# Kernel tuning notes

Measured on AMD Instinct MI355X. Metric: run time of the kernel, lower is better.

The kernel has to match this reference:

```python
import jax, jax.numpy as jnp
import numpy as np

BN_EPS = 1e-5
L2_EPS = 1e-12


def setup_inputs() -> dict:
    key = jax.random.key(0)
    ks = jax.random.split(key, 4)
    N, C = 524288, 32          # total points, FCGF feature dim
    L = 32768                  # points per cloud (segment length), B = N // L = 16
    K1, K2, FC = 128, 512, 256 # K_MLP = [128, 512], FC = [256]

    def lin(k, out_d, in_d):
        return jax.random.normal(k, (out_d, in_d), jnp.float32) * (1.0 / np.sqrt(in_d))

    return {
        "x": jax.random.normal(ks[0], (N, C), jnp.float32),
        "w1": lin(ks[1], K1, C),   "b1": jnp.zeros((K1,), jnp.float32),
        "g1": jnp.ones((K1,), jnp.float32), "be1": jnp.zeros((K1,), jnp.float32),
        "w2": lin(ks[2], K2, K1),  "b2": jnp.zeros((K2,), jnp.float32),
        "g2": jnp.ones((K2,), jnp.float32), "be2": jnp.zeros((K2,), jnp.float32),
        "wf": lin(ks[3], FC, C * K2), "bf": jnp.zeros((FC,), jnp.float32),
        "gf": jnp.ones((FC,), jnp.float32), "bef": jnp.zeros((FC,), jnp.float32),
        "seg_len": L,
    }


def _bn(h, g, b):
    # BatchNorm1d in training mode: per-channel batch stats (biased var),
    # reduction over all non-channel dims (here axis 0).
    mu = h.mean(axis=0, keepdims=True)
    var = h.var(axis=0, keepdims=True)
    return (h - mu) * jax.lax.rsqrt(var + BN_EPS) * g + b


def reference(x, w1, b1, g1, be1, w2, b2, g2, be2, wf, bf, gf, bef, seg_len):
    N = x.shape[0]
    B = N // seg_len
    # pointwise Conv1d == per-point Linear; BN over all N points per channel
    h = jax.nn.relu(_bn(x @ w1.T + b1, g1, be1))      # [N, 128]
    att = jax.nn.relu(_bn(h @ w2.T + b2, g2, be2))    # [N, 512]
    att_b = att.reshape(B, seg_len, att.shape[-1])    # [B, L, 512]
    x_b = x.reshape(B, seg_len, x.shape[-1])          # [B, L, 32]
    # per-segment attention-weighted pooling: att_i^T @ x_i / n_i
    pooled = jnp.einsum("blk,blc->bkc", att_b, x_b) / seg_len  # [B, 512, 32]
    gp = att_b.sum(axis=1)                            # [B, 512]
    res = _bn(pooled.reshape(B, -1) @ wf.T + bf, gf, bef)       # [B, 256]
    # F.normalize(p=2, dim=1)
    nrm = jnp.linalg.norm(res, axis=1, keepdims=True)
    res = res / jnp.maximum(nrm, L2_EPS)
    lengths = jnp.full((B, 1), seg_len, dtype=jnp.int32)
    return (res, gp, lengths)
```

## Files before the change

kernel.cpp:

```cpp
#include <hip/hip_runtime.h>
#include <hip/hip_bf16.h>


#define SEGLEN 32768
#define BN_EPS 1e-5f
#define INV_N (1.0f/524288.0f)
#define INV_L (1.0f/32768.0f)

#define WS_BIG   0
#define WS_TMPG  8650752
#define WS_S1    8782848
#define WS_G     8783904
#define WS_W1F   8800416
#define WS_B1P   8802464
#define WS_W2F   8802592
#define WS_B2P   8835360
#define WS_PR    8835872
#define WS_TP    9098016

typedef __attribute__((ext_vector_type(8))) short bf16x8;
typedef __attribute__((ext_vector_type(4))) float f32x4;
#define MFMA(a,b,c) __builtin_amdgcn_mfma_f32_16x16x32_bf16(a,b,c,0,0,0)

__device__ __forceinline__ unsigned short f2b(float f) {
    unsigned u = __builtin_bit_cast(unsigned, f);
    return (unsigned short)((u + 0x7FFFu + ((u >> 16) & 1u)) >> 16);
}
__device__ __forceinline__ unsigned cvtpk(float a, float b) {
    unsigned r;
    asm("v_cvt_pk_bf16_f32 %0, %1, %2" : "=v"(r) : "v"(a), "v"(b));
    return r;
}

__global__ __launch_bounds__(256) void k1_stats_x(const float* __restrict__ x,
                                                  float* __restrict__ part) {
    __shared__ float xs[64 * 36];
    const int tid = threadIdx.x;
    const int blk = blockIdx.x;
    const long base = (long)blk * 1024;
    float acc0 = 0.f, acc1 = 0.f, acc2 = 0.f, acc3 = 0.f;
    float sxa = 0.f;
    const int i0 = (tid * 4) >> 5;
    const int j0 = (tid * 4) & 31;
    const int sp0 = tid >> 3, sc4 = (tid & 7) * 4;
    float4 st0 = *(const float4*)&x[(base + sp0) * 32 + sc4];
    float4 st1 = *(const float4*)&x[(base + sp0 + 32) * 32 + sc4];
    for (int t0 = 0; t0 < 1024; t0 += 64) {
        __syncthreads();
        *(float4*)&xs[sp0 * 36 + sc4] = st0;
        *(float4*)&xs[(sp0 + 32) * 36 + sc4] = st1;
        if (t0 < 960) {
            st0 = *(const float4*)&x[(base + t0 + 64 + sp0) * 32 + sc4];
            st1 = *(const float4*)&x[(base + t0 + 64 + sp0 + 32) * 32 + sc4];
        }
        __syncthreads();
        #pragma unroll 8
        for (int p = 0; p < 64; p++) {
            float xi = xs[p * 36 + i0];
            float4 xj = *(float4*)&xs[p * 36 + j0];
            acc0 += xi * xj.x; acc1 += xi * xj.y;
            acc2 += xi * xj.z; acc3 += xi * xj.w;
        }
        if (tid < 32) {
            #pragma unroll 8
            for (int p = 0; p < 64; p++) sxa += xs[p * 36 + tid];
        }
    }
    float* dst = part + (long)blk * 1056;
    *(float4*)&dst[tid * 4] = make_float4(acc0, acc1, acc2, acc3);
    if (tid < 32) dst[1024 + tid] = sxa;
}

__global__ void k_reduceA(const float* __restrict__ in, float* __restrict__ out,
                          int npp, int nentries) {
    int e = blockIdx.x * 256 + threadIdx.x;
    if (e >= nentries) return;
    const float* src = in + (long)blockIdx.y * npp * nentries;
    float s = 0.f;
    #pragma unroll 8
    for (int p = 0; p < npp; p++) s += src[(long)p * nentries + e];
    out[(long)blockIdx.y * nentries + e] = s;
}

__global__ void k_reduce(const float* __restrict__ in, float* __restrict__ out,
                         int nparts, int nentries) {
    int e = blockIdx.x * 256 + threadIdx.x;
    if (e >= nentries) return;
    float s = 0.f;
    #pragma unroll 8
    for (int p = 0; p < nparts; p++) s += in[(long)p * nentries + e];
    out[e] = s;
}

__global__ __launch_bounds__(128) void k2_fold1(const float* __restrict__ S1,
                                                const float* __restrict__ w1,
                                                const float* __restrict__ b1,
                                                const float* __restrict__ g1,
                                                const float* __restrict__ be1,
                                                unsigned short* __restrict__ w1f,
                                                float* __restrict__ b1p) {
    __shared__ float s1[1056];
    const int k = threadIdx.x;
    for (int q = k; q < 1056; q += 128) s1[q] = S1[q];
    __syncthreads();
    float w[32];
    #pragma unroll
    for (int c = 0; c < 32; c++) w[c] = w1[k * 32 + c];
    float s = 0.f;
    #pragma unroll
    for (int c = 0; c < 32; c++) s += w[c] * s1[1024 + c];
    s *= INV_N;
    float q = 0.f;
    for (int i = 0; i < 32; i++) {
        float t = 0.f;
        #pragma unroll
        for (int j = 0; j < 32; j++) t += s1[i * 32 + j] * w[j];
        q += w[i] * t;
    }
    q *= INV_N;
    float var = q - s * s;
    float mu = s + b1[k];
    float a = g1[k] * rsqrtf(var + BN_EPS);
    #pragma unroll
    for (int c = 0; c < 32; c++) w1f[k * 32 + c] = f2b(a * w[c]);
    b1p[k] = a * (b1[k] - mu) + be1[k];
}

__global__ __launch_bounds__(512, 2) void kB_stats(const float* __restrict__ x,
                                                   const unsigned short* __restrict__ w1f,
                                                   const float* __restrict__ b1p,
                                                   float* __restrict__ gpart) {
    __shared__ unsigned short xsb[64 * 40];
    __shared__ unsigned short hT[128 * 72];
    __shared__ float shred[8 * 64];
    const int tid = threadIdx.x;
    const int wave = tid >> 6, lane = tid & 63;
    const int l15 = lane & 15, lg = lane >> 4;
    const int ptile = wave & 3, chalf = wave >> 2;
    const long base = (long)blockIdx.x * 1024;
    const f32x4 zero4 = {0.f, 0.f, 0.f, 0.f};
    bf16x8 wb1[4];
    f32x4 binit1[4];
    #pragma unroll
    for (int c = 0; c < 4; c++) {
        int ch = chalf * 64 + c * 16 + l15;
        wb1[c] = *(const bf16x8*)&w1f[ch * 32 + lg * 8];
        float b = b1p[ch];
        binit1[c] = (f32x4){b, b, b, b};
    }
    f32x4 gacc[8];
    #pragma unroll
    for (int t = 0; t < 8; t++) gacc[t] = zero4;
    float shacc[4] = {0.f, 0.f, 0.f, 0.f};
    const int sp = tid >> 3, sc4 = (tid & 7) * 4;
    float4 xsg = *(const float4*)&x[(base + sp) * 32 + sc4];
    for (int ck = 0; ck < 16; ck++) {
        __syncthreads();
        *(uint2*)&xsb[sp * 40 + sc4] =
            make_uint2(cvtpk(xsg.x, xsg.y), cvtpk(xsg.z, xsg.w));
        if (ck < 15)
            xsg = *(const float4*)&x[(base + (ck + 1) * 64 + sp) * 32 + sc4];
        __syncthreads();
        bf16x8 xa = *(const bf16x8*)&xsb[(ptile * 16 + l15) * 40 + lg * 8];
        #pragma unroll
        for (int c = 0; c < 4; c++) {
            f32x4 hf = MFMA(xa, wb1[c], binit1[c]);
            float v0 = fmaxf(hf[0], 0.f);
            float v1 = fmaxf(hf[1], 0.f);
            float v2 = fmaxf(hf[2], 0.f);
            float v3 = fmaxf(hf[3], 0.f);
            shacc[c] += (v0 + v1) + (v2 + v3);
            int ch = chalf * 64 + c * 16 + l15;
            *(uint2*)&hT[ch * 72 + ptile * 16 + lg * 4] =
                make_uint2(cvtpk(v0, v1), cvtpk(v2, v3));
        }
        __syncthreads();
        #pragma unroll
        for (int ks = 0; ks < 2; ks++) {
            bf16x8 ga = *(const bf16x8*)&hT[(wave * 16 + l15) * 72 + ks * 32 + lg * 8];
            #pragma unroll
            for (int ct = 0; ct < 8; ct++) {
                bf16x8 gb = *(const bf16x8*)&hT[(ct * 16 + l15) * 72 + ks * 32 + lg * 8];
                gacc[ct] = MFMA(ga, gb, gacc[ct]);
            }
        }
    }
    float* dst = gpart + (long)blockIdx.x * 16512;
    #pragma unroll
    for (int ct = 0; ct < 8; ct++) {
        #pragma unroll
        for (int r = 0; r < 4; r++)
            dst[(wave * 16 + lg * 4 + r) * 128 + ct * 16 + l15] = gacc[ct][r];
    }
    #pragma unroll
    for (int c = 0; c < 4; c++) {
        float v = shacc[c];
        v += __shfl_xor(v, 16);
        v += __shfl_xor(v, 32);
        if (lane < 16) shred[wave * 64 + c * 16 + lane] = v;
    }
    __syncthreads();
    if (tid < 128) {
        float s = 0.f;
        #pragma unroll
        for (int pt = 0; pt < 4; pt++)
            s += shred[((tid >> 6) * 4 + pt) * 64 + (tid & 63)];
        dst[16384 + tid] = s;
    }
}

__global__ __launch_bounds__(128) void k4_fold2(const float* __restrict__ G,
                                                const float* __restrict__ w2,
                                                const float* __restrict__ b2,
                                                const float* __restrict__ g2,
                                                const float* __restrict__ be2,
                                                unsigned short* __restrict__ w2f,
                                                float* __restrict__ b2p) {
    __shared__ float wsh[128];
    __shared__ float red[4];
    const int i = threadIdx.x;
    const int k = blockIdx.x;
    const float wi = w2[(long)k * 128 + i];
    wsh[i] = wi;
    __syncthreads();
    float t = 0.f;
    const float* grow = &G[i * 128];
    #pragma unroll 16
    for (int j = 0; j < 128; j++) t += grow[j] * wsh[j];
    float qp = wi * t;
    float sp = wi * G[16384 + i];
    #pragma unroll
    for (int o = 1; o < 64; o <<= 1) {
        qp += __shfl_xor(qp, o);
        sp += __shfl_xor(sp, o);
    }
    if ((i & 63) == 0) {
        red[(i >> 6) * 2 + 0] = qp;
        red[(i >> 6) * 2 + 1] = sp;
    }
    __syncthreads();
    const float q = (red[0] + red[2]) * INV_N;
    const float s = (red[1] + red[3]) * INV_N;
    const float var = q - s * s;
    const float a = g2[k] * rsqrtf(var + BN_EPS);
    w2f[(long)k * 128 + i] = f2b(a * wi);
    if (i == 0) b2p[k] = -a * s + be2[k];
}

__global__ __launch_bounds__(512, 2) void kD_main(const float* __restrict__ x,
        const unsigned short* __restrict__ w1f, const float* __restrict__ b1p,
        const unsigned short* __restrict__ w2f, const float* __restrict__ b2p,
        float* __restrict__ ppart) {
    __shared__ unsigned short xT[32 * 72];
    __shared__ unsigned short hs[64 * 136];
    __shared__ unsigned short attT[8][64 * 40];
    const int tid = threadIdx.x;
    const int wave = tid >> 6, lane = tid & 63;
    const int l15 = lane & 15, lg = lane >> 4;
    const int ptile = wave & 3, chalf = wave >> 2;
    const int kb = wave * 64;
    const long base = (long)blockIdx.x * 1024;
    const f32x4 zero4 = {0.f, 0.f, 0.f, 0.f};
    bf16x8 wb1[4];
    f32x4 binit1[4];
    #pragma unroll
    for (int c = 0; c < 4; c++) {
        int ch = chalf * 64 + c * 16 + l15;
        wb1[c] = *(const bf16x8*)&w1f[ch * 32 + lg * 8];
        float b = b1p[ch];
        binit1[c] = (f32x4){b, b, b, b};
    }
    bf16x8 wb2[4][4];
    f32x4 binit2[4];
    #pragma unroll
    for (int c = 0; c < 4; c++) {
        int ch = kb + c * 16 + l15;
        #pragma unroll
        for (int ks = 0; ks < 4; ks++)
            wb2[c][ks] = *(const bf16x8*)&w2f[(long)ch * 128 + ks * 32 + lg * 8];
        float b = b2p[ch];
        binit2[c] = (f32x4){b, b, b, b};
    }
    f32x4 pacc[4][2];
    #pragma unroll
    for (int t = 0; t < 4; t++) { pacc[t][0] = zero4; pacc[t][1] = zero4; }
    float gpacc[4] = {0.f, 0.f, 0.f, 0.f};
    const int sp = tid >> 3, sc4 = (tid & 7) * 4;
    const int hpt = ptile * 16 + l15;
    float4 xsg, xh0, xh1;
    xsg = *(const float4*)&x[(base + sp) * 32 + sc4];
    {
        const float* r = &x[(base + hpt) * 32 + lg * 8];
        xh0 = *(const float4*)&r[0];
        xh1 = *(const float4*)&r[4];
    }
    for (int ck = 0; ck < 16; ck++) {
        __syncthreads();
        {
            unsigned dxy = cvtpk(xsg.x, xsg.y);
            unsigned dzw = cvtpk(xsg.z, xsg.w);
            xT[(sc4 + 0) * 72 + sp] = (unsigned short)dxy;
            xT[(sc4 + 1) * 72 + sp] = (unsigned short)(dxy >> 16);
            xT[(sc4 + 2) * 72 + sp] = (unsigned short)dzw;
            xT[(sc4 + 3) * 72 + sp] = (unsigned short)(dzw >> 16);
        }
        {
            bf16x8 xa;
            ((unsigned*)&xa)[0] = cvtpk(xh0.x, xh0.y);
            ((unsigned*)&xa)[1] = cvtpk(xh0.z, xh0.w);
            ((unsigned*)&xa)[2] = cvtpk(xh1.x, xh1.y);
            ((unsigned*)&xa)[3] = cvtpk(xh1.z, xh1.w);
            #pragma unroll
            for (int c = 0; c < 4; c++) {
                f32x4 hf = MFMA(xa, wb1[c], binit1[c]);
                int chh = chalf * 64 + c * 16 + l15;
                int rb = ptile * 16 + lg * 4;
                unsigned d0 = cvtpk(fmaxf(hf[0], 0.f), fmaxf(hf[1], 0.f));
                unsigned d1 = cvtpk(fmaxf(hf[2], 0.f), fmaxf(hf[3], 0.f));
                hs[(rb + 0) * 136 + chh] = (unsigned short)d0;
                hs[(rb + 1) * 136 + chh] = (unsigned short)(d0 >> 16);
                hs[(rb + 2) * 136 + chh] = (unsigned short)d1;
                hs[(rb + 3) * 136 + chh] = (unsigned short)(d1 >> 16);
            }
        }
        if (ck < 15) {
            long nb = base + (ck + 1) * 64;
            xsg = *(const float4*)&x[(nb + sp) * 32 + sc4];
            const float* r = &x[(nb + hpt) * 32 + lg * 8];
            xh0 = *(const float4*)&r[0];
            xh1 = *(const float4*)&r[4];
        }
        __syncthreads();
        #pragma unroll
        for (int ph = 0; ph < 2; ph++) {
            f32x4 zt[2][4];
            #pragma unroll
            for (int r = 0; r < 2; r++) {
                zt[r][0] = binit2[0]; zt[r][1] = binit2[1];
                zt[r][2] = binit2[2]; zt[r][3] = binit2[3];
            }
            #pragma unroll
            for (int ks = 0; ks < 4; ks++) {
                bf16x8 ha[2];
                #pragma unroll
                for (int r = 0; r < 2; r++)
                    ha[r] = *(const bf16x8*)&hs[(ph * 32 + r * 16 + l15) * 136 + ks * 32 + lg * 8];
                #pragma unroll
                for (int r = 0; r < 2; r++)
                    #pragma unroll
                    for (int c = 0; c < 4; c++)
                        zt[r][c] = MFMA(ha[r], wb2[c][ks], zt[r][c]);
            }
            #pragma unroll
            for (int r = 0; r < 2; r++) {
                #pragma unroll
                for (int c = 0; c < 4; c++) {
                    float a0 = fmaxf(zt[r][c][0], 0.f);
                    float a1 = fmaxf(zt[r][c][1], 0.f);
                    float a2 = fmaxf(zt[r][c][2], 0.f);
                    float a3 = fmaxf(zt[r][c][3], 0.f);
                    gpacc[c] += (a0 + a1) + (a2 + a3);
                    *(uint2*)&attT[wave][(c * 16 + l15) * 40 + r * 16 + lg * 4] =
                        make_uint2(cvtpk(a0, a1), cvtpk(a2, a3));
                }
            }
            bf16x8 xb[2];
            #pragma unroll
            for (int u = 0; u < 2; u++)
                xb[u] = *(const bf16x8*)&xT[(u * 16 + l15) * 72 + ph * 32 + lg * 8];
            #pragma unroll
            for (int t = 0; t < 4; t++) {
                bf16x8 aa = *(const bf16x8*)&attT[wave][(t * 16 + l15) * 40 + lg * 8];
                #pragma unroll
                for (int u = 0; u < 2; u++)
                    pacc[t][u] = MFMA(aa, xb[u], pacc[t][u]);
            }
        }
    }
    float* dst = ppart + (long)blockIdx.x * 16896;
    #pragma unroll
    for (int t = 0; t < 4; t++)
        #pragma unroll
        for (int u = 0; u < 2; u++)
            #pragma unroll
            for (int r = 0; r < 4; r++)
                dst[(kb + t * 16 + lg * 4 + r) * 32 + u * 16 + l15] = pacc[t][u][r];
    #pragma unroll
    for (int c = 0; c < 4; c++) {
        float v = gpacc[c];
        v += __shfl_xor(v, 16);
        v += __shfl_xor(v, 32);
        if (lane < 16) dst[16384 + kb + c * 16 + lane] = v;
    }
}

__global__ void k5b_reduce_pool(const float* __restrict__ part,
                                float* __restrict__ pooled_red,
                                float* __restrict__ out) {
    const int seg = blockIdx.y;
    const int e = blockIdx.x * 256 + threadIdx.x;
    if (e >= 16896) return;
    float s = 0.f;
    #pragma unroll 8
    for (int p = 0; p < 32; p++)
        s += part[(long)(seg * 32 + p) * 16896 + e];
    if (e < 16384) pooled_red[seg * 16384 + e] = s;
    else out[4096 + seg * 512 + (e - 16384)] = s;
}

__global__ __launch_bounds__(256) void k6a_fc(const float* __restrict__ pr,
                                              const float* __restrict__ wf,
                                              float* __restrict__ tpart) {
    const int kbk = blockIdx.x, jb = blockIdx.y;
    const int j = jb * 16 + (threadIdx.x >> 4), b = threadIdx.x & 15;
    const float4* wrow = (const float4*)&wf[(long)j * 16384 + kbk * 1024];
    const float4* prow = (const float4*)&pr[(long)b * 16384 + kbk * 1024];
    float acc = 0.f;
    #pragma unroll 8
    for (int u = 0; u < 256; u++) {
        float4 w = wrow[u], p = prow[u];
        acc += w.x * p.x + w.y * p.y + w.z * p.z + w.w * p.w;
    }
    tpart[(kbk * 16 + b) * 256 + j] = acc;
}

__global__ __launch_bounds__(256) void k6b_final(const float* __restrict__ tpart,
                                                 const float* __restrict__ bf_,
                                                 const float* __restrict__ gf,
                                                 const float* __restrict__ bef,
                                                 float* __restrict__ out) {
    __shared__ float ts[16 * 256];
    __shared__ float rs[16 * 256];
    __shared__ float nrm[16];
    const int tid = threadIdx.x;
    for (int b = 0; b < 16; b++) {
        float s = 0.f;
        #pragma unroll
        for (int kbk = 0; kbk < 16; kbk++) s += tpart[(kbk * 16 + b) * 256 + tid];
        ts[b * 256 + tid] = s * INV_L + bf_[tid];
    }
    __syncthreads();
    float mu = 0.f;
    #pragma unroll
    for (int b = 0; b < 16; b++) mu += ts[b * 256 + tid];
    mu *= (1.f / 16.f);
    float var = 0.f;
    #pragma unroll
    for (int b = 0; b < 16; b++) {
        float d = ts[b * 256 + tid] - mu;
        var += d * d;
    }
    var *= (1.f / 16.f);
    float a = gf[tid] * rsqrtf(var + BN_EPS);
    #pragma unroll
    for (int b = 0; b < 16; b++)
        rs[b * 256 + tid] = (ts[b * 256 + tid] - mu) * a + bef[tid];
    __syncthreads();
    {
        const int pb = tid >> 4, l16 = tid & 15;
        float s = 0.f;
        #pragma unroll
        for (int j = 0; j < 16; j++) {
            float v = rs[pb * 256 + l16 + j * 16];
            s += v * v;
        }
        s += __shfl_xor(s, 1); s += __shfl_xor(s, 2);
        s += __shfl_xor(s, 4); s += __shfl_xor(s, 8);
        if (l16 == 0) nrm[pb] = fmaxf(sqrtf(s), 1e-12f);
    }
    __syncthreads();
    #pragma unroll
    for (int b = 0; b < 16; b++)
        out[b * 256 + tid] = rs[b * 256 + tid] / nrm[b];
    if (tid < 16) out[12288 + tid] = 32768.0f;
}

extern "C" void kernel_launch(void* const* d_in, const int* in_sizes, int n_in,
                              void* d_out, int out_size, void* d_ws, size_t ws_size,
                              hipStream_t stream) {
    (void)in_sizes; (void)n_in; (void)out_size; (void)ws_size;
    const float* x   = (const float*)d_in[0];
    const float* w1  = (const float*)d_in[1];
    const float* b1  = (const float*)d_in[2];
    const float* g1  = (const float*)d_in[3];
    const float* be1 = (const float*)d_in[4];
    const float* w2  = (const float*)d_in[5];
    const float* b2  = (const float*)d_in[6];
    const float* g2  = (const float*)d_in[7];
    const float* be2 = (const float*)d_in[8];
    const float* wf  = (const float*)d_in[9];
    const float* bf  = (const float*)d_in[10];
    const float* gf  = (const float*)d_in[11];
    const float* bef = (const float*)d_in[12];
    float* out = (float*)d_out;
    float* ws = (float*)d_ws;
    unsigned short* w1f = (unsigned short*)(ws + WS_W1F);
    unsigned short* w2f = (unsigned short*)(ws + WS_W2F);

    k1_stats_x<<<512, 256, 0, stream>>>(x, ws + WS_BIG);
    k_reduceA<<<dim3(5, 8), 256, 0, stream>>>(ws + WS_BIG, ws + WS_TMPG, 64, 1056);
    k_reduce<<<5, 256, 0, stream>>>(ws + WS_TMPG, ws + WS_S1, 8, 1056);
    k2_fold1<<<1, 128, 0, stream>>>(ws + WS_S1, w1, b1, g1, be1, w1f, ws + WS_B1P);
    kB_stats<<<512, 512, 0, stream>>>(x, w1f, ws + WS_B1P, ws + WS_BIG);
    k_reduceA<<<dim3(65, 8), 256, 0, stream>>>(ws + WS_BIG, ws + WS_TMPG, 64, 16512);
    k_reduce<<<65, 256, 0, stream>>>(ws + WS_TMPG, ws + WS_G, 8, 16512);
    k4_fold2<<<512, 128, 0, stream>>>(ws + WS_G, w2, b2, g2, be2, w2f, ws + WS_B2P);
    kD_main<<<512, 512, 0, stream>>>(x, w1f, ws + WS_B1P, w2f, ws + WS_B2P, ws + WS_BIG);
    k5b_reduce_pool<<<dim3(66, 16), 256, 0, stream>>>(ws + WS_BIG, ws + WS_PR, out);
    k6a_fc<<<dim3(16, 16), 256, 0, stream>>>(ws + WS_PR, wf, ws + WS_TP);
    k6b_final<<<1, 256, 0, stream>>>(ws + WS_TP, bf, gf, bef, out);
}
```

Before: 363.2 us.

## Swizzle LDS layouts with XOR and double points per block in main kernels

Replaces padded shared-memory rows (stride 72/136) with unpadded rows whose column index is XOR-swizzled by row, so reads and writes avoid bank conflicts and use less LDS. It also halves the grid of kB_stats and kD_main to 256 blocks, each handling 2048 points, and halves the number of partials to be reduced downstream. Fewer blocks means less occupancy on a large-CU GPU, traded against reduced partial-write and reduction traffic.

Result: slower. 384.8 us (+5.9%).

```diff
diff --git a/kernel.cpp b/kernel.cpp
--- a/kernel.cpp
+++ b/kernel.cpp
@@ -131,13 +131,14 @@
                                                    const float* __restrict__ b1p,
                                                    float* __restrict__ gpart) {
     __shared__ unsigned short xsb[64 * 40];
-    __shared__ unsigned short hT[128 * 72];
+    __shared__ unsigned short hT[128 * 64];
     __shared__ float shred[8 * 64];
     const int tid = threadIdx.x;
     const int wave = tid >> 6, lane = tid & 63;
     const int l15 = lane & 15, lg = lane >> 4;
     const int ptile = wave & 3, chalf = wave >> 2;
-    const long base = (long)blockIdx.x * 1024;
+    const int rx = (l15 & 7) << 3;
+    const long base = (long)blockIdx.x * 2048;
     const f32x4 zero4 = {0.f, 0.f, 0.f, 0.f};
     bf16x8 wb1[4];
     f32x4 binit1[4];
@@ -154,11 +155,11 @@
     float shacc[4] = {0.f, 0.f, 0.f, 0.f};
     const int sp = tid >> 3, sc4 = (tid & 7) * 4;
     float4 xsg = *(const float4*)&x[(base + sp) * 32 + sc4];
-    for (int ck = 0; ck < 16; ck++) {
+    for (int ck = 0; ck < 32; ck++) {
         __syncthreads();
         *(uint2*)&xsb[sp * 40 + sc4] =
             make_uint2(cvtpk(xsg.x, xsg.y), cvtpk(xsg.z, xsg.w));
-        if (ck < 15)
+        if (ck < 31)
             xsg = *(const float4*)&x[(base + (ck + 1) * 64 + sp) * 32 + sc4];
         __syncthreads();
         bf16x8 xa = *(const bf16x8*)&xsb[(ptile * 16 + l15) * 40 + lg * 8];
@@ -171,16 +172,16 @@
             float v3 = fmaxf(hf[3], 0.f);
             shacc[c] += (v0 + v1) + (v2 + v3);
             int ch = chalf * 64 + c * 16 + l15;
-            *(uint2*)&hT[ch * 72 + ptile * 16 + lg * 4] =
+            *(uint2*)&hT[ch * 64 + ((ptile * 16 + lg * 4) ^ rx)] =
                 make_uint2(cvtpk(v0, v1), cvtpk(v2, v3));
         }
         __syncthreads();
         #pragma unroll
         for (int ks = 0; ks < 2; ks++) {
-            bf16x8 ga = *(const bf16x8*)&hT[(wave * 16 + l15) * 72 + ks * 32 + lg * 8];
+            bf16x8 ga = *(const bf16x8*)&hT[(wave * 16 + l15) * 64 + ((ks * 32 + lg * 8) ^ rx)];
             #pragma unroll
             for (int ct = 0; ct < 8; ct++) {
-                bf16x8 gb = *(const bf16x8*)&hT[(ct * 16 + l15) * 72 + ks * 32 + lg * 8];
+                bf16x8 gb = *(const bf16x8*)&hT[(ct * 16 + l15) * 64 + ((ks * 32 + lg * 8) ^ rx)];
                 gacc[ct] = MFMA(ga, gb, gacc[ct]);
             }
         }
@@ -251,15 +252,16 @@
         const unsigned short* __restrict__ w1f, const float* __restrict__ b1p,
         const unsigned short* __restrict__ w2f, const float* __restrict__ b2p,
         float* __restrict__ ppart) {
-    __shared__ unsigned short xT[32 * 72];
-    __shared__ unsigned short hs[64 * 136];
+    __shared__ unsigned short xT[32 * 64];
+    __shared__ unsigned short hs[64 * 128];
     __shared__ unsigned short attT[8][64 * 40];
     const int tid = threadIdx.x;
     const int wave = tid >> 6, lane = tid & 63;
     const int l15 = lane & 15, lg = lane >> 4;
     const int ptile = wave & 3, chalf = wave >> 2;
     const int kb = wave * 64;
-    const long base = (long)blockIdx.x * 1024;
+    const int rx = (l15 & 7) << 3;
+    const long base = (long)blockIdx.x * 2048;
     const f32x4 zero4 = {0.f, 0.f, 0.f, 0.f};
     bf16x8 wb1[4];
     f32x4 binit1[4];
@@ -294,15 +296,15 @@
         xh0 = *(const float4*)&r[0];
         xh1 = *(const float4*)&r[4];
     }
-    for (int ck = 0; ck < 16; ck++) {
+    for (int ck = 0; ck < 32; ck++) {
         __syncthreads();
         {
             unsigned dxy = cvtpk(xsg.x, xsg.y);
             unsigned dzw = cvtpk(xsg.z, xsg.w);
-            xT[(sc4 + 0) * 72 + sp] = (unsigned short)dxy;
-            xT[(sc4 + 1) * 72 + sp] = (unsigned short)(dxy >> 16);
-            xT[(sc4 + 2) * 72 + sp] = (unsigned short)dzw;
-            xT[(sc4 + 3) * 72 + sp] = (unsigned short)(dzw >> 16);
+            xT[(sc4 + 0) * 64 + (sp ^ (((sc4 + 0) & 7) << 3))] = (unsigned short)dxy;
+            xT[(sc4 + 1) * 64 + (sp ^ (((sc4 + 1) & 7) << 3))] = (unsigned short)(dxy >> 16);
+            xT[(sc4 + 2) * 64 + (sp ^ (((sc4 + 2) & 7) << 3))] = (unsigned short)dzw;
+            xT[(sc4 + 3) * 64 + (sp ^ (((sc4 + 3) & 7) << 3))] = (unsigned short)(dzw >> 16);
         }
         {
             bf16x8 xa;
@@ -317,13 +319,13 @@
                 int rb = ptile * 16 + lg * 4;
                 unsigned d0 = cvtpk(fmaxf(hf[0], 0.f), fmaxf(hf[1], 0.f));
                 unsigned d1 = cvtpk(fmaxf(hf[2], 0.f), fmaxf(hf[3], 0.f));
-                hs[(rb + 0) * 136 + chh] = (unsigned short)d0;
-                hs[(rb + 1) * 136 + chh] = (unsigned short)(d0 >> 16);
-                hs[(rb + 2) * 136 + chh] = (unsigned short)d1;
-                hs[(rb + 3) * 136 + chh] = (unsigned short)(d1 >> 16);
+                hs[(rb + 0) * 128 + (chh ^ (((rb + 0) & 7) << 3))] = (unsigned short)d0;
+                hs[(rb + 1) * 128 + (chh ^ (((rb + 1) & 7) << 3))] = (unsigned short)(d0 >> 16);
+                hs[(rb + 2) * 128 + (chh ^ (((rb + 2) & 7) << 3))] = (unsigned short)d1;
+                hs[(rb + 3) * 128 + (chh ^ (((rb + 3) & 7) << 3))] = (unsigned short)(d1 >> 16);
             }
         }
-        if (ck < 15) {
+        if (ck < 31) {
             long nb = base + (ck + 1) * 64;
             xsg = *(const float4*)&x[(nb + sp) * 32 + sc4];
             const float* r = &x[(nb + hpt) * 32 + lg * 8];
@@ -344,7 +346,8 @@
                 bf16x8 ha[2];
                 #pragma unroll
                 for (int r = 0; r < 2; r++)
-                    ha[r] = *(const bf16x8*)&hs[(ph * 32 + r * 16 + l15) * 136 + ks * 32 + lg * 8];
+                    ha[r] = *(const bf16x8*)&hs[(ph * 32 + r * 16 + l15) * 128
+                                                + ((ks * 32 + lg * 8) ^ rx)];
                 #pragma unroll
                 for (int r = 0; r < 2; r++)
                     #pragma unroll
@@ -367,7 +370,8 @@
             bf16x8 xb[2];
             #pragma unroll
             for (int u = 0; u < 2; u++)
-                xb[u] = *(const bf16x8*)&xT[(u * 16 + l15) * 72 + ph * 32 + lg * 8];
+                xb[u] = *(const bf16x8*)&xT[(u * 16 + l15) * 64
+                                            + ((ph * 32 + lg * 8) ^ rx)];
             #pragma unroll
             for (int t = 0; t < 4; t++) {
                 bf16x8 aa = *(const bf16x8*)&attT[wave][(t * 16 + l15) * 40 + lg * 8];
@@ -401,9 +405,9 @@
     const int e = blockIdx.x * 256 + threadIdx.x;
     if (e >= 16896) return;
     float s = 0.f;
-    #pragma unroll 8
-    for (int p = 0; p < 32; p++)
-        s += part[(long)(seg * 32 + p) * 16896 + e];
+    #pragma unroll
+    for (int p = 0; p < 16; p++)
+        s += part[(long)(seg * 16 + p) * 16896 + e];
     if (e < 16384) pooled_red[seg * 16384 + e] = s;
     else out[4096 + seg * 512 + (e - 16384)] = s;
 }
@@ -501,11 +505,11 @@
     k_reduceA<<<dim3(5, 8), 256, 0, stream>>>(ws + WS_BIG, ws + WS_TMPG, 64, 1056);
     k_reduce<<<5, 256, 0, stream>>>(ws + WS_TMPG, ws + WS_S1, 8, 1056);
     k2_fold1<<<1, 128, 0, stream>>>(ws + WS_S1, w1, b1, g1, be1, w1f, ws + WS_B1P);
-    kB_stats<<<512, 512, 0, stream>>>(x, w1f, ws + WS_B1P, ws + WS_BIG);
-    k_reduceA<<<dim3(65, 8), 256, 0, stream>>>(ws + WS_BIG, ws + WS_TMPG, 64, 16512);
+    kB_stats<<<256, 512, 0, stream>>>(x, w1f, ws + WS_B1P, ws + WS_BIG);
+    k_reduceA<<<dim3(65, 8), 256, 0, stream>>>(ws + WS_BIG, ws + WS_TMPG, 32, 16512);
     k_reduce<<<65, 256, 0, stream>>>(ws + WS_TMPG, ws + WS_G, 8, 16512);
     k4_fold2<<<512, 128, 0, stream>>>(ws + WS_G, w2, b2, g2, be2, w2f, ws + WS_B2P);
-    kD_main<<<512, 512, 0, stream>>>(x, w1f, ws + WS_B1P, w2f, ws + WS_B2P, ws + WS_BIG);
+    kD_main<<<256, 512, 0, stream>>>(x, w1f, ws + WS_B1P, w2f, ws + WS_B2P, ws + WS_BIG);
     k5b_reduce_pool<<<dim3(66, 16), 256, 0, stream>>>(ws + WS_BIG, ws + WS_PR, out);
     k6a_fc<<<dim3(16, 16), 256, 0, stream>>>(ws + WS_PR, wf, ws + WS_TP);
     k6b_final<<<1, 256, 0, stream>>>(ws + WS_TP, bf, gf, bef, out);
```
